# Kernel optimization log

Hardware: AMD Instinct MI355X
Metric: run time of the kernel (lower is better)

Reference implementation:

```python
import jax, jax.numpy as jnp
import numpy as np

B, N, M, D, H = 16, 512, 8, 768, 12
Dh = D // H
SCALE = Dh ** -0.5


def setup_inputs() -> dict:
    key = jax.random.key(0)
    ks = jax.random.split(key, 8)
    w = 0.02  # init scale keeps logits well-conditioned
    return {
        "x": jax.random.normal(ks[0], (B, N, D), dtype=jnp.float32),
        "sim_embeddings": jax.random.normal(ks[1], (B, N, M, D), dtype=jnp.float32),
        "Wq": jax.random.normal(ks[2], (D, D), dtype=jnp.float32) * w,
        "bq": jnp.zeros((D,), dtype=jnp.float32),
        "Wkv": jax.random.normal(ks[3], (D, 2 * D), dtype=jnp.float32) * w,
        "bkv": jnp.zeros((2 * D,), dtype=jnp.float32),
        "Wp": jax.random.normal(ks[4], (D, D), dtype=jnp.float32) * w,
        "bp": jnp.zeros((D,), dtype=jnp.float32),
    }


def reference(x, sim_embeddings, Wq, bq, Wkv, bkv, Wp, bp):
    # q: (B,H,N,Dh)
    q = (x @ Wq + bq).reshape(B, N, H, Dh).transpose(0, 2, 1, 3)
    # self kv: (B,H,N,Dh) each
    kv = x @ Wkv + bkv
    k_x, v_x = jnp.split(kv, 2, axis=-1)
    k_x = k_x.reshape(B, N, H, Dh).transpose(0, 2, 1, 3)
    v_x = v_x.reshape(B, N, H, Dh).transpose(0, 2, 1, 3)
    # neighbor kv: (B,H,N,M,Dh) each
    kv_sim = sim_embeddings @ Wkv + bkv
    k_sim, v_sim = jnp.split(kv_sim, 2, axis=-1)
    k_sim = k_sim.reshape(B, N, M, H, Dh).transpose(0, 3, 1, 2, 4)
    v_sim = v_sim.reshape(B, N, M, H, Dh).transpose(0, 3, 1, 2, 4)
    # logits: self (B,H,N,N) concat per-query neighbor (B,H,N,M)
    logits_self = jnp.einsum("bhnd,bhmd->bhnm", q, k_x) * SCALE
    logits_sim = jnp.einsum("bhnd,bhnmd->bhnm", q, k_sim) * SCALE
    attn = jax.nn.softmax(jnp.concatenate([logits_self, logits_sim], axis=-1), axis=-1)
    attn_self, attn_sim = attn[..., :N], attn[..., N:]
    out_self = jnp.einsum("bhnm,bhmd->bhnd", attn_self, v_x)
    out_sim = jnp.einsum("bhnm,bhnmd->bhnd", attn_sim, v_sim)
    out = (out_self + out_sim).transpose(0, 2, 1, 3).reshape(B, N, D)
    return out @ Wp + bp
```

## Files before the change

### kernel.cpp

```cpp
#include <hip/hip_runtime.h>

typedef __bf16 bf16;
typedef __bf16 bf16x8 __attribute__((ext_vector_type(8)));
typedef __bf16 bf16x4 __attribute__((ext_vector_type(4)));
typedef float  f32x4  __attribute__((ext_vector_type(4)));

#define SCALE 0.125f

__device__ __forceinline__ void gl_lds16(const bf16* g, bf16* l) {
  __builtin_amdgcn_global_load_lds(
      (const __attribute__((address_space(1))) void*)g,
      (__attribute__((address_space(3))) void*)l, 16, 0, 0);
}

__global__ __launch_bounds__(256) void prep_all(
    const float* __restrict__ x, const float* __restrict__ Wq,
    const float* __restrict__ Wkv, const float* __restrict__ Wp,
    const float* __restrict__ bq, const float* __restrict__ bkv,
    bf16* __restrict__ xb, bf16* __restrict__ Wqkvt, bf16* __restrict__ Wpt,
    bf16* __restrict__ Wkvb, float* __restrict__ bias1) {
  int bid = blockIdx.x;
  if (bid < 6144) {
    int i = bid * 256 + threadIdx.x;
    float4 v = ((const float4*)x)[i];
    bf16x4 o = { (bf16)v.x, (bf16)v.y, (bf16)v.z, (bf16)v.w };
    *(bf16x4*)(xb + (size_t)i * 4) = o;
  } else if (bid < 7296) {
    int i = (bid - 6144) * 256 + threadIdx.x;
    float4 v = ((const float4*)Wkv)[i];
    bf16x4 o = { (bf16)v.x, (bf16)v.y, (bf16)v.z, (bf16)v.w };
    *(bf16x4*)(Wkvb + (size_t)i * 4) = o;
  } else {
    int idx = (bid - 7296) * 256 + threadIdx.x;
    const int T1 = 2304 * 768, T2 = 768 * 768;
    if (idx < T1) {
      int c = idx / 768, j = idx - c * 768;
      float v = (c < 768) ? Wq[(size_t)j * 768 + c] : Wkv[(size_t)j * 1536 + (c - 768)];
      Wqkvt[idx] = (bf16)v;
    } else if (idx < T1 + T2) {
      int t2 = idx - T1;
      int c = t2 / 768, j = t2 - c * 768;
      Wpt[t2] = (bf16)Wp[(size_t)j * 768 + c];
    } else if (idx < T1 + T2 + 2304) {
      int c = idx - T1 - T2;
      bias1[c] = (c < 768) ? bq[c] : bkv[c - 768];
    }
  }
}

__global__ __launch_bounds__(256) void gemm_bt(
    const bf16* __restrict__ A, const bf16* __restrict__ Bt,
    const float* __restrict__ bias,
    bf16* __restrict__ Cb, float* __restrict__ Cf,
    int Mdim, int Ndim, int Kdim) {
  __shared__ alignas(16) bf16 As[128 * 32];
  __shared__ alignas(16) bf16 Bs[128 * 32];
  int tid = threadIdx.x;
  int lane = tid & 63, wave = tid >> 6;
  int wr = wave >> 1, wc = wave & 1;
  int bm = blockIdx.y * 128, bn = blockIdx.x * 128;
  int lr = lane & 15, quad = lane >> 4;
  f32x4 acc[4][4] = {};
  for (int kb = 0; kb < Kdim; kb += 32) {
    __syncthreads();
#pragma unroll
    for (int i = 0; i < 2; i++) {
      int c = tid + i * 256;
      int r = c >> 2, cc = (c & 3) * 8;
      bf16* ldsbase_a = As + ((size_t)i * 256 + wave * 64) * 8;
      bf16* ldsbase_b = Bs + ((size_t)i * 256 + wave * 64) * 8;
      gl_lds16(A + (size_t)(bm + r) * Kdim + kb + cc, ldsbase_a);
      gl_lds16(Bt + (size_t)(bn + r) * Kdim + kb + cc, ldsbase_b);
    }
    __syncthreads();
    bf16x8 af[4], bg[4];
#pragma unroll
    for (int mi = 0; mi < 4; mi++)
      af[mi] = *(const bf16x8*)(As + (wr * 64 + mi * 16 + lr) * 32 + quad * 8);
#pragma unroll
    for (int ni = 0; ni < 4; ni++)
      bg[ni] = *(const bf16x8*)(Bs + (wc * 64 + ni * 16 + lr) * 32 + quad * 8);
#pragma unroll
    for (int mi = 0; mi < 4; mi++)
#pragma unroll
      for (int ni = 0; ni < 4; ni++)
        acc[mi][ni] = __builtin_amdgcn_mfma_f32_16x16x32_bf16(af[mi], bg[ni], acc[mi][ni], 0, 0, 0);
  }
#pragma unroll
  for (int mi = 0; mi < 4; mi++)
#pragma unroll
    for (int ni = 0; ni < 4; ni++)
#pragma unroll
      for (int r = 0; r < 4; r++) {
        int row = bm + wr * 64 + mi * 16 + quad * 4 + r;
        int col = bn + wc * 64 + ni * 16 + lr;
        float v = acc[mi][ni][r] + bias[col];
        if (Cb) Cb[(size_t)row * Ndim + col] = (bf16)v;
        else    Cf[(size_t)row * Ndim + col] = v;
      }
}

__global__ __launch_bounds__(256) void gemm_bt_g(
    const bf16* __restrict__ A, int lda, int aZ,
    const bf16* __restrict__ Bt, int ldb, int bZ,
    bf16* __restrict__ Cb, float* __restrict__ Cf, int ldc, int cZ,
    const float* __restrict__ bias, int biasZ,
    const float* __restrict__ rowscale, int rsLd,
    int Kdim) {
  __shared__ alignas(16) bf16 As[128 * 32];
  __shared__ alignas(16) bf16 Bs[64 * 32];
  int tid = threadIdx.x;
  int lane = tid & 63, wave = tid >> 6;
  int wr = wave >> 1, wc = wave & 1;
  int bm = blockIdx.y * 128, bn = blockIdx.x * 64;
  int z = blockIdx.z;
  const bf16* Ab = A + (size_t)z * aZ;
  const bf16* Bb = Bt + (size_t)z * bZ;
  int lr = lane & 15, quad = lane >> 4;
  f32x4 acc[4][2] = {};
  for (int kb = 0; kb < Kdim; kb += 32) {
    __syncthreads();
#pragma unroll
    for (int i = 0; i < 2; i++) {
      int c = tid + i * 256;
      int r = c >> 2, cc = (c & 3) * 8;
      gl_lds16(Ab + (size_t)(bm + r) * lda + kb + cc,
               As + ((size_t)i * 256 + wave * 64) * 8);
    }
    {
      int r = tid >> 2, cc = (tid & 3) * 8;
      gl_lds16(Bb + (size_t)(bn + r) * ldb + kb + cc,
               Bs + (size_t)(wave * 64) * 8);
    }
    __syncthreads();
    bf16x8 af[4], bg[2];
#pragma unroll
    for (int mi = 0; mi < 4; mi++)
      af[mi] = *(const bf16x8*)(As + (wr * 64 + mi * 16 + lr) * 32 + quad * 8);
#pragma unroll
    for (int ni = 0; ni < 2; ni++)
      bg[ni] = *(const bf16x8*)(Bs + (wc * 32 + ni * 16 + lr) * 32 + quad * 8);
#pragma unroll
    for (int mi = 0; mi < 4; mi++)
#pragma unroll
      for (int ni = 0; ni < 2; ni++)
        acc[mi][ni] = __builtin_amdgcn_mfma_f32_16x16x32_bf16(af[mi], bg[ni], acc[mi][ni], 0, 0, 0);
  }
#pragma unroll
  for (int mi = 0; mi < 4; mi++)
#pragma unroll
    for (int ni = 0; ni < 2; ni++)
#pragma unroll
      for (int r = 0; r < 4; r++) {
        int row = bm + wr * 64 + mi * 16 + quad * 4 + r;
        int col = wc * 32 + ni * 16 + lr;
        float v = acc[mi][ni][r];
        if (bias) {
          float sc = rowscale ? rowscale[(size_t)row * rsLd + z] : 1.f;
          v += bias[z * biasZ + col] * sc;
        }
        size_t idx = (size_t)row * ldc + (size_t)z * cZ + bn + col;
        if (Cb) Cb[idx] = (bf16)v;
        else    Cf[idx] = v;
      }
}

__global__ __launch_bounds__(256) void sim_logits(
    const float* __restrict__ sim,
    bf16* __restrict__ U,
    const bf16* __restrict__ qkv,
    const float* __restrict__ bias1,
    int bn0,
    float* __restrict__ msim, float* __restrict__ lsim) {
  __shared__ alignas(16) float simS[8][772];
  __shared__ alignas(16) bf16  uS[12][776];
  __shared__ float logitS[12][8];
  __shared__ float wS[12][8];
  __shared__ float cS[12];
  int t = threadIdx.x;
  int pair = blockIdx.x;
  int bn = bn0 + pair;
  const float4* s4 = (const float4*)(sim + (size_t)pair * 6144);
#pragma unroll
  for (int ii = 0; ii < 6; ii++) {
    int i = t + ii * 256;
    float4 v = s4[i];
    int m = i / 192, jj = (i - m * 192) * 4;
    *(float4*)(&simS[m][jj]) = v;
  }
  const int4* u4 = (const int4*)(U + (size_t)pair * 9216);
  for (int i = t; i < 1152; i += 256) {
    int h = i / 96, c8 = (i - h * 96) * 8;
    *(int4*)(&uS[h][c8]) = u4[i];
  }
  if (t < 96) {
    int h = t >> 3, d0 = (t & 7) * 8;
    bf16 qq[8];
    *(int4*)qq = *(const int4*)(qkv + (size_t)bn * 2304 + h * 64 + d0);
    float s = 0.f;
#pragma unroll
    for (int e = 0; e < 8; e++) s += (float)qq[e] * bias1[768 + h * 64 + d0 + e];
    s += __shfl_xor(s, 1, 64);
    s += __shfl_xor(s, 2, 64);
    s += __shfl_xor(s, 4, 64);
    if ((t & 7) == 0) cS[h] = s;
  }
  __syncthreads();
  if (t < 192) {
    int hm = t >> 1, half = t & 1;
    int h = hm >> 3, m = hm & 7;
    float s = 0.f;
#pragma unroll 8
    for (int kk = 0; kk < 48; kk++) {
      int j0 = kk * 16 + half * 8;
      bf16x8 uv = *(const bf16x8*)(&uS[h][j0]);
      float4 a = *(const float4*)(&simS[m][j0]);
      float4 b = *(const float4*)(&simS[m][j0 + 4]);
      s += a.x * (float)uv[0] + a.y * (float)uv[1] + a.z * (float)uv[2] + a.w * (float)uv[3]
         + b.x * (float)uv[4] + b.y * (float)uv[5] + b.z * (float)uv[6] + b.w * (float)uv[7];
    }
    s += __shfl_xor(s, 1, 64);
    if (!half) logitS[h][m] = (s + cS[h]) * SCALE;
  }
  __syncthreads();
  if (t < 12) {
    float mx = logitS[t][0];
#pragma unroll
    for (int m = 1; m < 8; m++) mx = fmaxf(mx, logitS[t][m]);
    float l = 0.f;
#pragma unroll
    for (int m = 0; m < 8; m++) { float e = __expf(logitS[t][m] - mx); wS[t][m] = e; l += e; }
    msim[(size_t)bn * 12 + t] = mx;
    lsim[(size_t)bn * 12 + t] = l;
  }
  __syncthreads();
  bf16* Sw = U + (size_t)pair * 9216;
  for (int i = t; i < 4608; i += 256) {
    int h = i / 384, j2 = (i - h * 384) * 2;
    float s0 = 0.f, s1 = 0.f;
#pragma unroll
    for (int m = 0; m < 8; m++) {
      float w = wS[h][m];
      s0 += w * simS[m][j2];
      s1 += w * simS[m][j2 + 1];
    }
    bf16 pr[2] = { (bf16)s0, (bf16)s1 };
    *(unsigned*)(&Sw[(size_t)h * 768 + j2]) = *(unsigned*)pr;
  }
}

__global__ __launch_bounds__(256) void self_attn(
    const bf16* __restrict__ qkv,
    const float* __restrict__ msim, const float* __restrict__ lsim,
    const float* __restrict__ osim,
    bf16* __restrict__ attn_out) {
  __shared__ alignas(16) bf16 Ks[128][72];
  __shared__ alignas(16) bf16 Vt[64][136];
  __shared__ alignas(16) bf16 Ps[4][16][136];
  int bid = blockIdx.x;
  int qc = bid & 7;
  int h  = (bid >> 3) % 12;
  int b  = bid / 96;
  int rowbase = b * 512;
  int q0 = qc * 64;
  int t = threadIdx.x, lane = t & 63, wv = t >> 6;
  int lr = lane & 15, quad = lane >> 4;

  const bf16* qrow = qkv + (size_t)(rowbase + q0 + wv * 16 + lr) * 2304 + h * 64;
  bf16x8 aq0 = *(const bf16x8*)(qrow + quad * 8);
  bf16x8 aq1 = *(const bf16x8*)(qrow + 32 + quad * 8);

  f32x4 oacc[4] = {};
  float mrow[4], lrow[4];
#pragma unroll
  for (int r = 0; r < 4; r++) { mrow[r] = -1e30f; lrow[r] = 0.f; }

  for (int kt = 0; kt < 4; kt++) {
    int jb = kt * 128;
    __syncthreads();
    for (int ci = t; ci < 1024; ci += 256) {
      int j = ci >> 3, off = (ci & 7) * 8;
      *(int4*)(&Ks[j][off]) =
          *(const int4*)(qkv + (size_t)(rowbase + jb + j) * 2304 + 768 + h * 64 + off);
    }
    for (int ci = t; ci < 512; ci += 256) {
      int jp = ci >> 3, off = (ci & 7) * 8;
      const bf16* v0 = qkv + (size_t)(rowbase + jb + jp * 2) * 2304 + 1536 + h * 64 + off;
      bf16 ta[8], tb[8];
      *(int4*)ta = *(const int4*)v0;
      *(int4*)tb = *(const int4*)(v0 + 2304);
#pragma unroll
      for (int e = 0; e < 8; e++) {
        bf16 pr[2] = { ta[e], tb[e] };
        *(unsigned*)(&Vt[off + e][jp * 2]) = *(unsigned*)pr;
      }
    }
    __syncthreads();

    f32x4 sacc[8] = {};
#pragma unroll
    for (int ni = 0; ni < 8; ni++) {
      int jj = ni * 16 + lr;
      bf16x8 bk0 = *(const bf16x8*)(&Ks[jj][quad * 8]);
      bf16x8 bk1 = *(const bf16x8*)(&Ks[jj][32 + quad * 8]);
      sacc[ni] = __builtin_amdgcn_mfma_f32_16x16x32_bf16(aq0, bk0, sacc[ni], 0, 0, 0);
      sacc[ni] = __builtin_amdgcn_mfma_f32_16x16x32_bf16(aq1, bk1, sacc[ni], 0, 0, 0);
    }
    float tm[4];
#pragma unroll
    for (int r = 0; r < 4; r++) {
      float v = sacc[0][r];
#pragma unroll
      for (int ni = 1; ni < 8; ni++) v = fmaxf(v, sacc[ni][r]);
      tm[r] = v;
    }
#pragma unroll
    for (int s = 1; s < 16; s <<= 1)
#pragma unroll
      for (int r = 0; r < 4; r++) tm[r] = fmaxf(tm[r], __shfl_xor(tm[r], s, 64));
    float alpha[4], s4[4];
#pragma unroll
    for (int r = 0; r < 4; r++) {
      float mnew = fmaxf(mrow[r], tm[r] * SCALE);
      alpha[r] = __expf(mrow[r] - mnew);
      mrow[r] = mnew;
      s4[r] = 0.f;
    }
#pragma unroll
    for (int ni = 0; ni < 8; ni++)
#pragma unroll
      for (int r = 0; r < 4; r++) {
        float p = __expf(sacc[ni][r] * SCALE - mrow[r]);
        s4[r] += p;
        Ps[wv][quad * 4 + r][ni * 16 + lr] = (bf16)p;
      }
#pragma unroll
    for (int s = 1; s < 16; s <<= 1)
#pragma unroll
      for (int r = 0; r < 4; r++) s4[r] += __shfl_xor(s4[r], s, 64);
#pragma unroll
    for (int r = 0; r < 4; r++) lrow[r] = lrow[r] * alpha[r] + s4[r];
#pragma unroll
    for (int ni = 0; ni < 4; ni++)
#pragma unroll
      for (int r = 0; r < 4; r++) oacc[ni][r] *= alpha[r];

#pragma unroll
    for (int kb = 0; kb < 4; kb++) {
      bf16x8 ap = *(const bf16x8*)(&Ps[wv][lr][kb * 32 + quad * 8]);
#pragma unroll
      for (int ni = 0; ni < 4; ni++) {
        bf16x8 bv = *(const bf16x8*)(&Vt[ni * 16 + lr][kb * 32 + quad * 8]);
        oacc[ni] = __builtin_amdgcn_mfma_f32_16x16x32_bf16(ap, bv, oacc[ni], 0, 0, 0);
      }
    }
  }

#pragma unroll
  for (int r = 0; r < 4; r++) {
    int bnI = rowbase + q0 + wv * 16 + quad * 4 + r;
    float ms = msim[(size_t)bnI * 12 + h], ls = lsim[(size_t)bnI * 12 + h];
    float mt = fmaxf(mrow[r], ms);
    float ea = __expf(mrow[r] - mt), eb = __expf(ms - mt);
    float inv = 1.f / (lrow[r] * ea + ls * eb);
#pragma unroll
    for (int ni = 0; ni < 4; ni++) {
      int d = ni * 16 + lr;
      float val = (oacc[ni][r] * ea + osim[(size_t)bnI * 768 + h * 64 + d] * eb) * inv;
      attn_out[(size_t)bnI * 768 + h * 64 + d] = (bf16)val;
    }
  }
}

extern "C" void kernel_launch(void* const* d_in, const int* in_sizes, int n_in,
                              void* d_out, int out_size, void* d_ws, size_t ws_size,
                              hipStream_t stream) {
  const float* x   = (const float*)d_in[0];
  const float* sim = (const float*)d_in[1];
  const float* Wq  = (const float*)d_in[2];
  const float* bq  = (const float*)d_in[3];
  const float* Wkv = (const float*)d_in[4];
  const float* bkv = (const float*)d_in[5];
  const float* Wp  = (const float*)d_in[6];
  const float* bp  = (const float*)d_in[7];
  float* out = (float*)d_out;

  char* ws = (char*)d_ws;
  size_t off = 0;
  auto carve = [&](size_t bytes) -> char* {
    char* p = ws + off;
    off = (off + bytes + 255) & ~(size_t)255;
    return p;
  };
  bf16*  xb    = (bf16*) carve((size_t)8192 * 768 * 2);
  bf16*  Wqkvt = (bf16*) carve((size_t)2304 * 768 * 2);
  bf16*  Wpt   = (bf16*) carve((size_t)768 * 768 * 2);
  bf16*  Wkvb  = (bf16*) carve((size_t)768 * 1536 * 2);
  float* bias1 = (float*)carve(2304 * 4);
  bf16*  qkv   = (bf16*) carve((size_t)8192 * 2304 * 2);
  float* msim  = (float*)carve((size_t)8192 * 12 * 4);
  float* lsim  = (float*)carve((size_t)8192 * 12 * 4);
  float* osim  = (float*)carve((size_t)8192 * 768 * 4);
  bf16*  attn  = (bf16*) carve((size_t)8192 * 768 * 2);
  size_t rem = (ws_size > off) ? ws_size - off : 0;
  int CH = 8192;
  while (CH > 128 && (size_t)CH * 18432 > rem) CH >>= 1;
  bf16* U = (bf16*)carve((size_t)CH * 12 * 768 * 2);

  prep_all<<<16521, 256, 0, stream>>>(x, Wq, Wkv, Wp, bq, bkv, xb, Wqkvt, Wpt, Wkvb, bias1);
  gemm_bt<<<dim3(18, 64), 256, 0, stream>>>(xb, Wqkvt, bias1, qkv, nullptr, 8192, 2304, 768);

  int nch = 8192 / CH;
  for (int c = 0; c < nch; c++) {
    int p0 = c * CH;
    gemm_bt_g<<<dim3(12, CH / 128, 12), 256, 0, stream>>>(
        qkv + (size_t)p0 * 2304, 2304, 64,
        Wkvb, 1536, 64,
        U, nullptr, 9216, 768,
        nullptr, 0, nullptr, 0, 64);
    sim_logits<<<CH, 256, 0, stream>>>(sim + (size_t)p0 * 6144, U, qkv, bias1, p0, msim, lsim);
    gemm_bt_g<<<dim3(1, CH / 128, 12), 256, 0, stream>>>(
        U, 9216, 768,
        Wqkvt + (size_t)1536 * 768, 768, 64 * 768,
        nullptr, osim + (size_t)p0 * 768, 768, 64,
        bias1 + 1536, 64, lsim + (size_t)p0 * 12, 12, 768);
  }
  self_attn<<<1536, 256, 0, stream>>>(qkv, msim, lsim, osim, attn);
  gemm_bt<<<dim3(6, 64), 256, 0, stream>>>(attn, Wpt, bp, nullptr, out, 8192, 768, 768);
}
```

Baseline: 621.2 us.

## Rewrite sim_logits with one wave per pair and MFMA for logits and weighted sum

```diff
diff --git a/kernel.cpp b/kernel.cpp
--- a/kernel.cpp
+++ b/kernel.cpp
@@ -172,80 +172,86 @@
     const float* __restrict__ bias1,
     int bn0,
     float* __restrict__ msim, float* __restrict__ lsim) {
-  __shared__ alignas(16) float simS[8][772];
-  __shared__ alignas(16) bf16  uS[12][776];
-  __shared__ float logitS[12][8];
-  __shared__ float wS[12][8];
-  __shared__ float cS[12];
-  int t = threadIdx.x;
-  int pair = blockIdx.x;
+  __shared__ bf16  simT[4][768][8];
+  __shared__ float wS[4][16][8];
+  int t = threadIdx.x, lane = t & 63, wv = t >> 6;
+  int pair = blockIdx.x * 4 + wv;
   int bn = bn0 + pair;
-  const float4* s4 = (const float4*)(sim + (size_t)pair * 6144);
-#pragma unroll
-  for (int ii = 0; ii < 6; ii++) {
-    int i = t + ii * 256;
-    float4 v = s4[i];
-    int m = i / 192, jj = (i - m * 192) * 4;
-    *(float4*)(&simS[m][jj]) = v;
-  }
-  const int4* u4 = (const int4*)(U + (size_t)pair * 9216);
-  for (int i = t; i < 1152; i += 256) {
-    int h = i / 96, c8 = (i - h * 96) * 8;
-    *(int4*)(&uS[h][c8]) = u4[i];
-  }
-  if (t < 96) {
-    int h = t >> 3, d0 = (t & 7) * 8;
-    bf16 qq[8];
-    *(int4*)qq = *(const int4*)(qkv + (size_t)bn * 2304 + h * 64 + d0);
-    float s = 0.f;
-#pragma unroll
-    for (int e = 0; e < 8; e++) s += (float)qq[e] * bias1[768 + h * 64 + d0 + e];
-    s += __shfl_xor(s, 1, 64);
-    s += __shfl_xor(s, 2, 64);
-    s += __shfl_xor(s, 4, 64);
-    if ((t & 7) == 0) cS[h] = s;
-  }
-  __syncthreads();
-  if (t < 192) {
-    int hm = t >> 1, half = t & 1;
-    int h = hm >> 3, m = hm & 7;
-    float s = 0.f;
-#pragma unroll 8
-    for (int kk = 0; kk < 48; kk++) {
-      int j0 = kk * 16 + half * 8;
-      bf16x8 uv = *(const bf16x8*)(&uS[h][j0]);
-      float4 a = *(const float4*)(&simS[m][j0]);
-      float4 b = *(const float4*)(&simS[m][j0 + 4]);
-      s += a.x * (float)uv[0] + a.y * (float)uv[1] + a.z * (float)uv[2] + a.w * (float)uv[3]
-         + b.x * (float)uv[4] + b.y * (float)uv[5] + b.z * (float)uv[6] + b.w * (float)uv[7];
-    }
-    s += __shfl_xor(s, 1, 64);
-    if (!half) logitS[h][m] = (s + cS[h]) * SCALE;
-  }
-  __syncthreads();
-  if (t < 12) {
-    float mx = logitS[t][0];
-#pragma unroll
-    for (int m = 1; m < 8; m++) mx = fmaxf(mx, logitS[t][m]);
-    float l = 0.f;
-#pragma unroll
-    for (int m = 0; m < 8; m++) { float e = __expf(logitS[t][m] - mx); wS[t][m] = e; l += e; }
-    msim[(size_t)bn * 12 + t] = mx;
-    lsim[(size_t)bn * 12 + t] = l;
-  }
-  __syncthreads();
-  bf16* Sw = U + (size_t)pair * 9216;
-  for (int i = t; i < 4608; i += 256) {
-    int h = i / 384, j2 = (i - h * 384) * 2;
-    float s0 = 0.f, s1 = 0.f;
-#pragma unroll
-    for (int m = 0; m < 8; m++) {
-      float w = wS[h][m];
-      s0 += w * simS[m][j2];
-      s1 += w * simS[m][j2 + 1];
-    }
-    bf16 pr[2] = { (bf16)s0, (bf16)s1 };
-    *(unsigned*)(&Sw[(size_t)h * 768 + j2]) = *(unsigned*)pr;
+  int lr = lane & 15, quad = lane >> 4;
+  int mrow = lane & 7;
+  int ur = lr < 12 ? lr : 11;
+
+  const float* simp = sim + (size_t)pair * 6144;
+  bf16* Up = U + (size_t)pair * 9216;
+
+  float cpart = 0.f;
+  {
+    int hh = lane >> 2, d0 = (lane & 3) * 16;
+    if (hh < 12) {
+      const bf16* qq = qkv + (size_t)bn * 2304 + hh * 64 + d0;
+      const float* bb = bias1 + 768 + hh * 64 + d0;
+#pragma unroll
+      for (int e = 0; e < 16; e++) cpart += (float)qq[e] * bb[e];
+    }
+    cpart += __shfl_xor(cpart, 1, 64);
+    cpart += __shfl_xor(cpart, 2, 64);
+  }
+  float ch = __shfl(cpart, ur << 2, 64);
+
+  f32x4 acc = {};
+  bool wlds = !(lane & 8);
+  for (int kb = 0; kb < 768; kb += 32) {
+    int j0 = kb + quad * 8;
+    float4 a0 = *(const float4*)(simp + (size_t)mrow * 768 + j0);
+    float4 a1 = *(const float4*)(simp + (size_t)mrow * 768 + j0 + 4);
+    bf16x8 af = { (bf16)a0.x, (bf16)a0.y, (bf16)a0.z, (bf16)a0.w,
+                  (bf16)a1.x, (bf16)a1.y, (bf16)a1.z, (bf16)a1.w };
+    if (wlds) {
+      int g = (j0 >> 3) & 3;
+#pragma unroll
+      for (int e = 0; e < 8; e++)
+        simT[wv][j0 + (e ^ g)][mrow] = af[e];
+    }
+    bf16x8 bf = *(const bf16x8*)(Up + (size_t)ur * 768 + j0);
+    acc = __builtin_amdgcn_mfma_f32_16x16x32_bf16(af, bf, acc, 0, 0, 0);
+  }
+  float s[4], mx = -1e30f;
+#pragma unroll
+  for (int r = 0; r < 4; r++) { s[r] = (acc[r] + ch) * SCALE; mx = fmaxf(mx, s[r]); }
+  mx = fmaxf(mx, __shfl_xor(mx, 16, 64));
+  float lsum = 0.f, w4[4];
+#pragma unroll
+  for (int r = 0; r < 4; r++) { w4[r] = __expf(s[r] - mx); lsum += w4[r]; }
+  lsum += __shfl_xor(lsum, 16, 64);
+  if (lane < 12) {
+    msim[(size_t)bn * 12 + lane] = mx;
+    lsim[(size_t)bn * 12 + lane] = lsum;
+  }
+  if (quad < 2 && lr < 12) {
+#pragma unroll
+    for (int r = 0; r < 4; r++) wS[wv][lr][quad * 4 + r] = w4[r];
+  }
+
+  bf16x8 aw = {};
+  if (quad == 0) {
+    const float* wrow = &wS[wv][ur][0];
+#pragma unroll
+    for (int e = 0; e < 8; e++) aw[e] = (bf16)wrow[e];
+  }
+  for (int j0 = 0; j0 < 768; j0 += 16) {
+    bf16x8 bs = {};
+    if (quad == 0) {
+      int j = j0 + lr;
+      int js = j ^ ((j >> 3) & 3);
+      bs = *(const bf16x8*)(&simT[wv][js][0]);
+    }
+    f32x4 o = {};
+    o = __builtin_amdgcn_mfma_f32_16x16x32_bf16(aw, bs, o, 0, 0, 0);
+    if (quad < 3) {
+#pragma unroll
+      for (int r = 0; r < 4; r++)
+        Up[(size_t)(quad * 4 + r) * 768 + j0 + lr] = (bf16)o[r];
+    }
   }
 }
 
@@ -418,7 +424,7 @@
         Wkvb, 1536, 64,
         U, nullptr, 9216, 768,
         nullptr, 0, nullptr, 0, 64);
-    sim_logits<<<CH, 256, 0, stream>>>(sim + (size_t)p0 * 6144, U, qkv, bias1, p0, msim, lsim);
+    sim_logits<<<CH / 4, 256, 0, stream>>>(sim + (size_t)p0 * 6144, U, qkv, bias1, p0, msim, lsim);
     gemm_bt_g<<<dim3(1, CH / 128, 12), 256, 0, stream>>>(
         U, 9216, 768,
         Wqkvt + (size_t)1536 * 768, 768, 64 * 768,
```

Measured after the change: 612.1 us. Within noise of the previous version (-1.5%).
